# Optimization experiments

Hardware: AMD Instinct MI355X
Metric: run time of the kernel (lower is better)

The kernel has to match this reference:

```python
import jax, jax.numpy as jnp
import numpy as np

SIGMA = 1.0  # RBF kernel bandwidth (init kwarg)

def setup_inputs() -> dict:
    key = jax.random.key(0)
    ks = jax.random.split(key, 5)
    B, N, D_in, D_emb = 8, 2048, 1024, 512
    scale = 1.0 / np.sqrt(D_in)
    return {
        "x": jax.random.normal(ks[0], (B, N, D_in), jnp.float32),
        "W_mu": jax.random.normal(ks[1], (D_emb, D_in), jnp.float32) * scale,
        "b_mu": jax.random.normal(ks[2], (D_emb,), jnp.float32) * scale,
        "W_logvar": jax.random.normal(ks[3], (D_emb, D_in), jnp.float32) * scale,
        "b_logvar": jax.random.normal(ks[4], (D_emb,), jnp.float32) * scale,
    }

def reference(x, W_mu, b_mu, W_logvar, b_logvar):
    # dual linear heads: (B,N,D_in) -> (B,N,D_emb)
    mu = jnp.einsum('bnd,ed->bne', x, W_mu) + b_mu
    logvar = jnp.einsum('bnd,ed->bne', x, W_logvar) + b_logvar
    sigma = jnp.exp(0.5 * logvar)
    # RBF kernel matrix K(x, x): (B,N,N) via ||xi||^2 + ||xj||^2 - 2 xi.xj
    sq = jnp.sum(x * x, axis=-1)                       # (B,N)
    gram = jnp.einsum('bnd,bmd->bnm', x, x)            # (B,N,N)
    dist = sq[:, :, None] + sq[:, None, :] - 2.0 * gram
    K = jnp.exp(-dist / (2.0 * SIGMA ** 2))            # (B,N,N)
    cov_diag = jnp.diagonal(K, axis1=1, axis2=2)       # (B,N) == exp(0) = 1
    sigma_adjusted = sigma * cov_diag[..., None]       # (B,N,D_emb)
    return (mu, sigma_adjusted)
```

## Files before the change

### kernel.cpp

```cpp
#include <hip/hip_runtime.h>
#include <hip/hip_bf16.h>
#include <math.h>

typedef __bf16 bf16;
typedef __attribute__((ext_vector_type(4))) float f32x4;
typedef __attribute__((ext_vector_type(8))) bf16 bf16x8;

#define M_TOT 16384
#define K_TOT 1024
#define D_EMB 512
#define NT 32

__global__ __launch_bounds__(256) void cvt_w_img(
    const float* __restrict__ W_mu, const float* __restrict__ W_logvar,
    bf16* __restrict__ img)
{
    const int c  = blockIdx.x * 256 + threadIdx.x;
    const int l  = c & 63;
    const int kt = (c >> 6) & 31;
    const int es = c >> 11;
    const int col = es * 16 + (l & 15);
    const int k0  = kt * 32 + (l >> 4) * 8;
    const float* s = (col < D_EMB) ? (W_mu + (size_t)col * K_TOT + k0)
                                   : (W_logvar + (size_t)(col - D_EMB) * K_TOT + k0);
    f32x4 a = ((const f32x4*)s)[0];
    f32x4 b = ((const f32x4*)s)[1];
    bf16x8 o;
    o[0] = (bf16)a[0]; o[1] = (bf16)a[1]; o[2] = (bf16)a[2]; o[3] = (bf16)a[3];
    o[4] = (bf16)b[0]; o[5] = (bf16)b[1]; o[6] = (bf16)b[2]; o[7] = (bf16)b[3];
    *(bf16x8*)(img + (size_t)c * 8) = o;
}

__global__ __launch_bounds__(512, 4) void gpe_gemm(
    const float* __restrict__ x,
    const bf16* __restrict__ wimg,
    const float* __restrict__ b_mu,
    const float* __restrict__ b_logvar,
    float* __restrict__ out)
{
    __shared__ __align__(16) bf16 Alds[2 * 128 * 32];

    const int tid  = threadIdx.x;
    const int lane = tid & 63;
    const int wid  = tid >> 6;
    const int wr   = wid >> 2;
    const int wc   = wid & 3;

    const int bid = blockIdx.x;
    const int swz = (bid & 7) * 64 + (bid >> 3);
    const int bn  = swz & 3;
    const int bm  = swz >> 2;

    const int r_l = tid >> 2;
    const int q   = tid & 3;
    const float* __restrict__ Asrc = x + (size_t)(bm * 128 + r_l) * K_TOT + q * 8;
    const int woff = r_l * 32 + ((q ^ ((r_l >> 1) & 3)) << 3);

    const int fr  = lane & 15;
    const int g16 = lane >> 4;

    const bf16* __restrict__ bb =
        wimg + (size_t)(bn * 16 + wc * 4) * 16384 + lane * 8;

    f32x4 acc[4][4];
#pragma unroll
    for (int m = 0; m < 4; ++m)
#pragma unroll
        for (int n = 0; n < 4; ++n)
            acc[m][n] = (f32x4){0.f, 0.f, 0.f, 0.f};

    f32x4 regA[2];
    bf16x8 bv[4];

    auto gloadA = [&](int t) {
        regA[0] = *(const f32x4*)(Asrc + t * 32);
        regA[1] = *(const f32x4*)(Asrc + t * 32 + 4);
    };
    auto cwA = [&](bf16* abase) {
        bf16x8 w;
#pragma unroll
        for (int j = 0; j < 4; ++j) { w[j] = (bf16)regA[0][j]; w[j + 4] = (bf16)regA[1][j]; }
        *(bf16x8*)&abase[woff] = w;
    };
    auto gloadB = [&](int t) {
#pragma unroll
        for (int n = 0; n < 4; ++n)
            bv[n] = *(const bf16x8*)(bb + (size_t)n * 16384 + t * 512);
    };

    gloadA(0);
    asm volatile("s_waitcnt vmcnt(0)" ::: "memory");
    cwA(Alds);
    gloadA(1);
    gloadB(0);
    asm volatile("s_waitcnt lgkmcnt(0)" ::: "memory");
    __builtin_amdgcn_s_barrier();

    for (int t = 0; t < NT; ++t) {
        const int p = t & 1;
        bf16* Ab  = Alds + p * 4096;
        bf16* Abn = Alds + (p ^ 1) * 4096;

        asm volatile("s_waitcnt vmcnt(0)" ::: "memory");
        if (t + 1 < NT) {
            cwA(Abn);
            if (t + 2 < NT) gloadA(t + 2);
        }

        bf16x8 af[4];
#pragma unroll
        for (int m = 0; m < 4; ++m) {
            const int row = wr * 64 + m * 16 + fr;
            af[m] = *(const bf16x8*)&Ab[row * 32 + ((g16 ^ ((row >> 1) & 3)) << 3)];
        }
        asm volatile("s_waitcnt lgkmcnt(0)" ::: "memory");
        __builtin_amdgcn_s_barrier();

        __builtin_amdgcn_s_setprio(1);
#pragma unroll
        for (int n = 0; n < 4; ++n)
#pragma unroll
            for (int m = 0; m < 4; ++m)
                acc[m][n] = __builtin_amdgcn_mfma_f32_16x16x32_bf16(af[m], bv[n], acc[m][n], 0, 0, 0);
        __builtin_amdgcn_s_setprio(0);

        if (t + 1 < NT) gloadB(t + 1);
    }

    const bool is_mu = (bn < 2);
    const float* __restrict__ bias = is_mu ? b_mu : b_logvar;
    const int cb = (bn & 1) * 256;
    float* __restrict__ obase = is_mu ? out : (out + (size_t)M_TOT * D_EMB);

#pragma unroll
    for (int m = 0; m < 4; ++m) {
        const int row0 = bm * 128 + wr * 64 + m * 16 + g16 * 4;
#pragma unroll
        for (int n = 0; n < 4; ++n) {
            const int c = cb + wc * 64 + n * 16 + fr;
            const float bvs = bias[c];
#pragma unroll
            for (int j = 0; j < 4; ++j) {
                float v = acc[m][n][j] + bvs;
                if (!is_mu) v = __expf(0.5f * v);
                obase[(size_t)(row0 + j) * D_EMB + c] = v;
            }
        }
    }
}

#define LDS_STRIDE 40
__global__ __launch_bounds__(256) void gpe_gemm_fb(
    const float* __restrict__ x, const float* __restrict__ W_mu,
    const float* __restrict__ b_mu, const float* __restrict__ W_logvar,
    const float* __restrict__ b_logvar, float* __restrict__ out)
{
    __shared__ __align__(16) bf16 As[128][LDS_STRIDE];
    __shared__ __align__(16) bf16 Bs[128][LDS_STRIDE];
    typedef __attribute__((ext_vector_type(4))) bf16 bf16x4;
    const int tid = threadIdx.x, lane = tid & 63, wid = tid >> 6;
    const int wr = wid >> 1, wc = wid & 1;
    const int bn = blockIdx.x & 7, bm = blockIdx.x >> 3;
    const int ebase = bn * 128;
    const bool is_mu = (ebase < D_EMB);
    const float* Wp = is_mu ? (W_mu + (size_t)ebase * K_TOT)
                            : (W_logvar + (size_t)(ebase - D_EMB) * K_TOT);
    const float* bias = is_mu ? b_mu : b_logvar;
    const int cbase = is_mu ? ebase : (ebase - D_EMB);
    float* obase = is_mu ? out : (out + (size_t)M_TOT * D_EMB);
    const float* Ap = x + (size_t)(bm * 128) * K_TOT;
    f32x4 acc[4][4];
#pragma unroll
    for (int m = 0; m < 4; ++m)
#pragma unroll
        for (int n = 0; n < 4; ++n) acc[m][n] = (f32x4){0.f, 0.f, 0.f, 0.f};
    const int fr = lane & 15, fk = (lane >> 4) * 8;
    const int arow = wr * 64 + fr, brow = wc * 64 + fr;
    for (int kt = 0; kt < K_TOT / 32; ++kt) {
        const int k0 = kt * 32;
#pragma unroll
        for (int s = 0; s < 4; ++s) {
            const int idx = s * 256 + tid;
            const int row = idx >> 3, col = (idx & 7) << 2;
            f32x4 va = *reinterpret_cast<const f32x4*>(Ap + (size_t)row * K_TOT + k0 + col);
            f32x4 vb = *reinterpret_cast<const f32x4*>(Wp + (size_t)row * K_TOT + k0 + col);
            bf16x4 ha, hb;
#pragma unroll
            for (int j = 0; j < 4; ++j) { ha[j] = (bf16)va[j]; hb[j] = (bf16)vb[j]; }
            *reinterpret_cast<bf16x4*>(&As[row][col]) = ha;
            *reinterpret_cast<bf16x4*>(&Bs[row][col]) = hb;
        }
        __syncthreads();
        bf16x8 af[4], bfv[4];
#pragma unroll
        for (int m = 0; m < 4; ++m)
            af[m] = *reinterpret_cast<const bf16x8*>(&As[arow + m * 16][fk]);
#pragma unroll
        for (int n = 0; n < 4; ++n)
            bfv[n] = *reinterpret_cast<const bf16x8*>(&Bs[brow + n * 16][fk]);
#pragma unroll
        for (int m = 0; m < 4; ++m)
#pragma unroll
            for (int n = 0; n < 4; ++n)
                acc[m][n] = __builtin_amdgcn_mfma_f32_16x16x32_bf16(af[m], bfv[n], acc[m][n], 0, 0, 0);
        __syncthreads();
    }
#pragma unroll
    for (int m = 0; m < 4; ++m) {
        const int rbase = bm * 128 + wr * 64 + m * 16 + (lane >> 4) * 4;
#pragma unroll
        for (int n = 0; n < 4; ++n) {
            const int c = cbase + wc * 64 + n * 16 + (lane & 15);
            const float bv = bias[c];
#pragma unroll
            for (int j = 0; j < 4; ++j) {
                float v = acc[m][n][j] + bv;
                if (!is_mu) v = __expf(0.5f * v);
                obase[(size_t)(rbase + j) * D_EMB + c] = v;
            }
        }
    }
}

extern "C" void kernel_launch(void* const* d_in, const int* in_sizes, int n_in,
                              void* d_out, int out_size, void* d_ws, size_t ws_size,
                              hipStream_t stream) {
    const float* x        = (const float*)d_in[0];
    const float* W_mu     = (const float*)d_in[1];
    const float* b_mu     = (const float*)d_in[2];
    const float* W_logvar = (const float*)d_in[3];
    const float* b_logvar = (const float*)d_in[4];
    float* out = (float*)d_out;

    const size_t ws_needed = (size_t)1024 * 1024 * sizeof(bf16);

    if (ws_size >= ws_needed) {
        bf16* wimg = (bf16*)d_ws;
        cvt_w_img<<<512, 256, 0, stream>>>(W_mu, W_logvar, wimg);
        gpe_gemm<<<512, 512, 0, stream>>>(x, wimg, b_mu, b_logvar, out);
    } else {
        gpe_gemm_fb<<<1024, 256, 0, stream>>>(x, W_mu, b_mu, W_logvar, b_logvar, out);
    }
}
```

Before: 51.84 us.

## Drop LDS staging for A and enlarge block tile to 256x256

Each wave now loads its A rows straight from global memory into registers and converts them to bf16 in registers, so the LDS double buffer and the per-step block barriers are gone. The block tile doubles to 256 rows by 256 columns: eight waves in a 4x2 layout, each computing 64x128 with 8 B fragments, and the grid drops to 256 blocks. This aims to cut LDS traffic and synchronisation and raise MFMA work per B load. In exchange, the two waves that share a row range both fetch the same A data through the caches, each CU holds fewer resident waves to hide latency, and the register footprint grows.

```diff
diff --git a/kernel.cpp b/kernel.cpp
--- a/kernel.cpp
+++ b/kernel.cpp
@@ -31,100 +31,85 @@
     *(bf16x8*)(img + (size_t)c * 8) = o;
 }
 
-__global__ __launch_bounds__(512, 4) void gpe_gemm(
+__global__ __launch_bounds__(512, 2) void gpe_gemm(
     const float* __restrict__ x,
     const bf16* __restrict__ wimg,
     const float* __restrict__ b_mu,
     const float* __restrict__ b_logvar,
     float* __restrict__ out)
 {
-    __shared__ __align__(16) bf16 Alds[2 * 128 * 32];
-
     const int tid  = threadIdx.x;
     const int lane = tid & 63;
     const int wid  = tid >> 6;
-    const int wr   = wid >> 2;
-    const int wc   = wid & 3;
+    const int wr   = wid >> 1;
+    const int wc   = wid & 1;
 
     const int bid = blockIdx.x;
-    const int swz = (bid & 7) * 64 + (bid >> 3);
+    const int swz = (bid & 7) * 32 + (bid >> 3);
     const int bn  = swz & 3;
     const int bm  = swz >> 2;
 
-    const int r_l = tid >> 2;
-    const int q   = tid & 3;
-    const float* __restrict__ Asrc = x + (size_t)(bm * 128 + r_l) * K_TOT + q * 8;
-    const int woff = r_l * 32 + ((q ^ ((r_l >> 1) & 3)) << 3);
-
     const int fr  = lane & 15;
     const int g16 = lane >> 4;
 
+    const float* __restrict__ Abase =
+        x + (size_t)(bm * 256 + wr * 64 + fr) * K_TOT + g16 * 8;
+
     const bf16* __restrict__ bb =
-        wimg + (size_t)(bn * 16 + wc * 4) * 16384 + lane * 8;
-
-    f32x4 acc[4][4];
+        wimg + (size_t)(bn * 16 + wc * 8) * 16384 + lane * 8;
+
+    f32x4 acc[4][8];
 #pragma unroll
     for (int m = 0; m < 4; ++m)
 #pragma unroll
-        for (int n = 0; n < 4; ++n)
+        for (int n = 0; n < 8; ++n)
             acc[m][n] = (f32x4){0.f, 0.f, 0.f, 0.f};
 
-    f32x4 regA[2];
-    bf16x8 bv[4];
-
-    auto gloadA = [&](int t) {
-        regA[0] = *(const f32x4*)(Asrc + t * 32);
-        regA[1] = *(const f32x4*)(Asrc + t * 32 + 4);
+    f32x4  pfA[8];
+    bf16x8 afc[4];
+    bf16x8 bv[8];
+
+    auto loadA = [&](int t) {
+#pragma unroll
+        for (int m = 0; m < 4; ++m) {
+            const float* p = Abase + (size_t)m * 16 * K_TOT + t * 32;
+            pfA[2 * m]     = *(const f32x4*)p;
+            pfA[2 * m + 1] = *(const f32x4*)(p + 4);
+        }
     };
-    auto cwA = [&](bf16* abase) {
-        bf16x8 w;
-#pragma unroll
-        for (int j = 0; j < 4; ++j) { w[j] = (bf16)regA[0][j]; w[j + 4] = (bf16)regA[1][j]; }
-        *(bf16x8*)&abase[woff] = w;
-    };
-    auto gloadB = [&](int t) {
-#pragma unroll
-        for (int n = 0; n < 4; ++n)
+    auto loadB = [&](int t) {
+#pragma unroll
+        for (int n = 0; n < 8; ++n)
             bv[n] = *(const bf16x8*)(bb + (size_t)n * 16384 + t * 512);
     };
-
-    gloadA(0);
-    asm volatile("s_waitcnt vmcnt(0)" ::: "memory");
-    cwA(Alds);
-    gloadA(1);
-    gloadB(0);
-    asm volatile("s_waitcnt lgkmcnt(0)" ::: "memory");
-    __builtin_amdgcn_s_barrier();
+    auto cvtA = [&]() {
+#pragma unroll
+        for (int m = 0; m < 4; ++m) {
+            bf16x8 w;
+#pragma unroll
+            for (int j = 0; j < 4; ++j) {
+                w[j]     = (bf16)pfA[2 * m][j];
+                w[j + 4] = (bf16)pfA[2 * m + 1][j];
+            }
+            afc[m] = w;
+        }
+    };
+
+    loadA(0);
+    loadB(0);
 
     for (int t = 0; t < NT; ++t) {
-        const int p = t & 1;
-        bf16* Ab  = Alds + p * 4096;
-        bf16* Abn = Alds + (p ^ 1) * 4096;
-
-        asm volatile("s_waitcnt vmcnt(0)" ::: "memory");
-        if (t + 1 < NT) {
-            cwA(Abn);
-            if (t + 2 < NT) gloadA(t + 2);
-        }
-
-        bf16x8 af[4];
-#pragma unroll
-        for (int m = 0; m < 4; ++m) {
-            const int row = wr * 64 + m * 16 + fr;
-            af[m] = *(const bf16x8*)&Ab[row * 32 + ((g16 ^ ((row >> 1) & 3)) << 3)];
-        }
-        asm volatile("s_waitcnt lgkmcnt(0)" ::: "memory");
-        __builtin_amdgcn_s_barrier();
-
+        cvtA();
+        if (t + 1 < NT) loadA(t + 1);
         __builtin_amdgcn_s_setprio(1);
 #pragma unroll
-        for (int n = 0; n < 4; ++n)
+        for (int n = 0; n < 8; ++n)
 #pragma unroll
             for (int m = 0; m < 4; ++m)
-                acc[m][n] = __builtin_amdgcn_mfma_f32_16x16x32_bf16(af[m], bv[n], acc[m][n], 0, 0, 0);
+                acc[m][n] = __builtin_amdgcn_mfma_f32_16x16x32_bf16(
+                    afc[m], bv[n], acc[m][n], 0, 0, 0);
         __builtin_amdgcn_s_setprio(0);
-
-        if (t + 1 < NT) gloadB(t + 1);
+        if (t + 1 < NT) loadB(t + 1);
     }
 
     const bool is_mu = (bn < 2);
@@ -134,10 +119,10 @@
 
 #pragma unroll
     for (int m = 0; m < 4; ++m) {
-        const int row0 = bm * 128 + wr * 64 + m * 16 + g16 * 4;
-#pragma unroll
-        for (int n = 0; n < 4; ++n) {
-            const int c = cb + wc * 64 + n * 16 + fr;
+        const int row0 = bm * 256 + wr * 64 + m * 16 + g16 * 4;
+#pragma unroll
+        for (int n = 0; n < 8; ++n) {
+            const int c = cb + wc * 128 + n * 16 + fr;
             const float bvs = bias[c];
 #pragma unroll
             for (int j = 0; j < 4; ++j) {
@@ -237,7 +222,7 @@
     if (ws_size >= ws_needed) {
         bf16* wimg = (bf16*)d_ws;
         cvt_w_img<<<512, 256, 0, stream>>>(W_mu, W_logvar, wimg);
-        gpe_gemm<<<512, 512, 0, stream>>>(x, wimg, b_mu, b_logvar, out);
+        gpe_gemm<<<256, 512, 0, stream>>>(x, wimg, b_mu, b_logvar, out);
     } else {
         gpe_gemm_fb<<<1024, 256, 0, stream>>>(x, W_mu, b_mu, W_logvar, b_logvar, out);
     }
```

Result: slower. 87.98 us (+69.7%).
